# Kernel optimization log

Hardware: AMD Instinct MI355X
Metric: run time of the kernel (lower is better)

The kernel has to match this reference:

```python
import jax, jax.numpy as jnp
import numpy as np

B, N, C, H, K = 16, 2048, 64, 128, 16
EPS = 1e-5  # torch BatchNorm1d default eps


def _bn(h, g, b, axes):
    # training-mode batch norm: biased variance over all non-channel axes
    m = h.mean(axes, keepdims=True)
    v = h.var(axes, keepdims=True)
    return (h - m) * jax.lax.rsqrt(v + EPS) * g + b


def _edge_conv(x, W1, b1, g1, be1, W2, b2, g2, be2):
    # x: [B, N, C]; dynamic kNN graph in feature space (per graph), includes self
    sq = jnp.sum(x * x, axis=-1)                                   # [B, N]
    d2 = sq[:, :, None] + sq[:, None, :] - 2.0 * jnp.einsum('bnc,bmc->bnm', x, x)
    idx = jax.lax.top_k(-d2, K)[1]                                 # [B, N, K]
    xj = jax.vmap(lambda xb, ib: xb[ib])(x, idx)                   # [B, N, K, C]
    xi = jnp.broadcast_to(x[:, :, None, :], xj.shape)
    h = jnp.concatenate([xi, xj - xi], axis=-1) @ W1 + b1          # [B, N, K, H]
    h = jax.nn.relu(_bn(h, g1, be1, (0, 1, 2)))
    h = h @ W2 + b2
    h = jax.nn.relu(_bn(h, g2, be2, (0, 1, 2)))
    return h.max(axis=2)                                           # max aggregation -> [B, N, H]


def setup_inputs() -> dict:
    key = jax.random.key(0)
    ks = jax.random.split(key, 8)
    inp = {
        'x': jax.random.normal(ks[0], (B * N, C), jnp.float32),
        'batch': jnp.repeat(jnp.arange(B, dtype=jnp.int32), N),
    }
    i = 1
    for pref in ('s', 't'):
        inp[f'{pref}_W1'] = jax.random.normal(ks[i], (2 * C, H), jnp.float32) * 0.05; i += 1
        inp[f'{pref}_b1'] = jnp.zeros((H,), jnp.float32)
        inp[f'{pref}_g1'] = jnp.ones((H,), jnp.float32)
        inp[f'{pref}_be1'] = jnp.zeros((H,), jnp.float32)
        inp[f'{pref}_W2'] = jax.random.normal(ks[i], (H, H), jnp.float32) * 0.05; i += 1
        inp[f'{pref}_b2'] = jnp.zeros((H,), jnp.float32)
        inp[f'{pref}_g2'] = jnp.ones((H,), jnp.float32)
        inp[f'{pref}_be2'] = jnp.zeros((H,), jnp.float32)
    inp['f_W'] = jax.random.normal(ks[i], (2 * H, H), jnp.float32) * 0.05
    inp['f_b'] = jnp.zeros((H,), jnp.float32)
    inp['f_g'] = jnp.ones((H,), jnp.float32)
    inp['f_be'] = jnp.zeros((H,), jnp.float32)
    return inp


def reference(x, batch,
              s_W1, s_b1, s_g1, s_be1, s_W2, s_b2, s_g2, s_be2,
              t_W1, t_b1, t_g1, t_be1, t_W2, t_b2, t_g2, t_be2,
              f_W, f_b, f_g, f_be):
    # batch is sorted with B equal-size graphs of N nodes -> reshape
    xb = x.reshape(B, N, C)
    xs = _edge_conv(xb, s_W1, s_b1, s_g1, s_be1, s_W2, s_b2, s_g2, s_be2)
    xt = _edge_conv(xb, t_W1, t_b1, t_g1, t_be1, t_W2, t_b2, t_g2, t_be2)
    comb = jnp.concatenate([xs, xt], axis=-1).reshape(B * N, 2 * H)
    h = comb @ f_W + f_b
    return jax.nn.relu(_bn(h, f_g, f_be, (0,)))
```

## Files before the change

### kernel.cpp

```cpp
#include <hip/hip_runtime.h>
#include <hip/hip_bf16.h>
#include <stdint.h>

#define NB 16
#define NN 2048
#define NC 64
#define NH 128
#define NK 16
#define NS (NB*NN)
#define NSK (NS*NK)
#define EPSV 1e-5f

typedef __attribute__((ext_vector_type(8))) short short8;
typedef __attribute__((ext_vector_type(8))) _Float16 half8;
typedef __attribute__((ext_vector_type(8))) unsigned short ushort8;
typedef __attribute__((ext_vector_type(4))) float f32x4;

__device__ __forceinline__ unsigned short f2bf(float x) {
  union { float f; unsigned u; } v; v.f = x;
  unsigned r = v.u + 0x7fffu + ((v.u >> 16) & 1u);
  return (unsigned short)(r >> 16);
}

__device__ __forceinline__ unsigned orderf(float f) {
  unsigned u = __float_as_uint(f);
  return u ^ ((unsigned)((int)u >> 31) | 0x80000000u);
}

__device__ __forceinline__ unsigned long long shfl_xor_u64(unsigned long long v, int m) {
  unsigned lo = (unsigned)(v & 0xffffffffull);
  unsigned hi = (unsigned)(v >> 32);
  lo = __shfl_xor(lo, m, 64);
  hi = __shfl_xor(hi, m, 64);
  return (((unsigned long long)hi) << 32) | lo;
}

__global__ void prep_x(const float* __restrict__ x, float* __restrict__ sq,
                       unsigned short* __restrict__ xh, unsigned short* __restrict__ xl) {
  int i = blockIdx.x * blockDim.x + threadIdx.x;
  if (i >= NS) return;
  const float4* x4 = (const float4*)(x + (size_t)i * NC);
  float s = 0.f;
#pragma unroll
  for (int k = 0; k < 8; k++) {
    float4 a = x4[2*k], b = x4[2*k+1];
    float f[8] = {a.x,a.y,a.z,a.w,b.x,b.y,b.z,b.w};
    ushort8 hv, lv;
#pragma unroll
    for (int j = 0; j < 8; j++) {
      float v = f[j];
      s += v*v;
      _Float16 h = (_Float16)v;
      float r = v - (float)h;
      _Float16 l = (_Float16)r;
      union { _Float16 ff; unsigned short u; } ch, cl;
      ch.ff = h; cl.ff = l;
      hv[j] = ch.u; lv[j] = cl.u;
    }
    *(ushort8*)(xh + (size_t)i*64 + k*8) = hv;
    *(ushort8*)(xl + (size_t)i*64 + k*8) = lv;
  }
  sq[i] = s;
}

__global__ __launch_bounds__(256) void knn5_kernel(const unsigned short* __restrict__ xh,
                                                   const unsigned short* __restrict__ xl,
                                                   const float* __restrict__ sq,
                                                   int* __restrict__ nbr) {
  __shared__ unsigned short rAh[64*64], rAl[64*64];
  __shared__ unsigned short cBh[64*64], cBl[64*64];
  __shared__ float sqc[64];
  __shared__ float d2s[256*17];
  int b = blockIdx.x >> 5;
  int rb = blockIdx.x & 31;
  int w = threadIdx.x >> 6, lane = threadIdx.x & 63;
  int n16 = lane & 15, q = lane >> 4;
  int rowbase = b*NN + rb*64;
  float* myd2 = &d2s[threadIdx.x * 17];

  {
    int r = threadIdx.x >> 2;
    int c0 = (threadIdx.x & 3) * 2;
#pragma unroll
    for (int cc = 0; cc < 2; cc++) {
      int c = c0 + cc;
      int pos = (c ^ (r & 7)) * 8;
      *(ushort8*)&rAh[r*64 + pos] = *(const ushort8*)(xh + (size_t)(rowbase + r)*64 + c*8);
      *(ushort8*)&rAl[r*64 + pos] = *(const ushort8*)(xl + (size_t)(rowbase + r)*64 + c*8);
    }
  }
  __syncthreads();
  half8 bh[2], bl[2];
  int m = w*16 + n16;
#pragma unroll
  for (int ks = 0; ks < 2; ks++) {
    int pos = ((ks*4 + q) ^ (m & 7)) * 8;
    bh[ks] = *(const half8*)&rAh[m*64 + pos];
    bl[ks] = *(const half8*)&rAl[m*64 + pos];
  }
  float sqr = sq[rowbase + m];

  unsigned long long keys[16];
#pragma unroll
  for (int i = 0; i < 16; i++) keys[i] = ~0ull;
  float wd2 = __builtin_inff();

  for (int ch = 0; ch < 32; ch++) {
    int colbase = b*NN + ch*64;
    __syncthreads();
    {
      int r = threadIdx.x >> 2;
      int c0 = (threadIdx.x & 3) * 2;
#pragma unroll
      for (int cc = 0; cc < 2; cc++) {
        int c = c0 + cc;
        int pos = (c ^ (r & 7)) * 8;
        *(ushort8*)&cBh[r*64 + pos] = *(const ushort8*)(xh + (size_t)(colbase + r)*64 + c*8);
        *(ushort8*)&cBl[r*64 + pos] = *(const ushort8*)(xl + (size_t)(colbase + r)*64 + c*8);
      }
      if (threadIdx.x < 64) sqc[threadIdx.x] = sq[colbase + threadIdx.x];
    }
    __syncthreads();
    f32x4 acc[4];
#pragma unroll
    for (int ci = 0; ci < 4; ci++) acc[ci] = (f32x4){0.f,0.f,0.f,0.f};
#pragma unroll
    for (int ks = 0; ks < 2; ks++) {
#pragma unroll
      for (int ci = 0; ci < 4; ci++) {
        int n = ci*16 + n16;
        int pos = ((ks*4 + q) ^ (n & 7)) * 8;
        half8 ah_ = *(const half8*)&cBh[n*64 + pos];
        half8 al_ = *(const half8*)&cBl[n*64 + pos];
        acc[ci] = __builtin_amdgcn_mfma_f32_16x16x32_f16(ah_, bh[ks], acc[ci], 0, 0, 0);
        acc[ci] = __builtin_amdgcn_mfma_f32_16x16x32_f16(al_, bh[ks], acc[ci], 0, 0, 0);
        acc[ci] = __builtin_amdgcn_mfma_f32_16x16x32_f16(ah_, bl[ks], acc[ci], 0, 0, 0);
      }
    }
    unsigned mask = 0;
#pragma unroll
    for (int ci = 0; ci < 4; ci++)
#pragma unroll
      for (int r = 0; r < 4; r++) {
        int idx = ci*4 + r;
        float d2 = fmaf(-2.f, acc[ci][r], sqr + sqc[ci*16 + q*4 + r]);
        myd2[idx] = d2;
        mask |= (d2 <= wd2) ? (1u << idx) : 0u;
      }
    while (mask) {
      int i = __builtin_ctz(mask);
      mask &= mask - 1;
      float dd = myd2[i];
      if (dd > wd2) continue;
      int col = colbase + (i >> 2)*16 + q*4 + (i & 3);
      unsigned long long key = ((unsigned long long)orderf(dd) << 32) | (unsigned)col;
#pragma unroll
      for (int j = 0; j < 16; j++) {
        bool cl = key < keys[j];
        unsigned long long lo = cl ? key : keys[j];
        key = cl ? keys[j] : key;
        keys[j] = lo;
      }
      unsigned whi = (unsigned)(keys[15] >> 32);
      wd2 = (whi == 0xffffffffu) ? __builtin_inff()
          : __uint_as_float((whi & 0x80000000u) ? (whi ^ 0x80000000u) : ~whi);
    }
  }
  for (int j = 0; j < NK; j++) {
    unsigned long long mk = keys[0];
#pragma unroll
    for (int i = 1; i < 16; i++) mk = (keys[i] < mk) ? keys[i] : mk;
    unsigned long long o = shfl_xor_u64(mk, 16); mk = (o < mk) ? o : mk;
    o = shfl_xor_u64(mk, 32); mk = (o < mk) ? o : mk;
#pragma unroll
    for (int i = 0; i < 16; i++) if (keys[i] == mk) keys[i] = ~0ull;
    if (q == 0) nbr[(size_t)(rowbase + m)*NK + j] = (int)(mk & 0xffffffffu);
  }
}

__global__ void prep_weights(const float* __restrict__ sW1, const float* __restrict__ sW2,
                             const float* __restrict__ tW1, const float* __restrict__ tW2,
                             const float* __restrict__ fW,
                             unsigned short* __restrict__ sW1t, unsigned short* __restrict__ sW2t,
                             unsigned short* __restrict__ tW1t, unsigned short* __restrict__ tW2t,
                             unsigned short* __restrict__ fWt) {
  int i = blockIdx.x * blockDim.x + threadIdx.x;
  if (i < 4*16384) {
    int mi = i >> 14, e = i & 16383;
    int h = e >> 7, k = e & 127;
    const float* src = (mi==0) ? sW1 : (mi==1) ? sW2 : (mi==2) ? tW1 : tW2;
    unsigned short* dst = (mi==0) ? sW1t : (mi==1) ? sW2t : (mi==2) ? tW1t : tW2t;
    dst[h*128 + k] = f2bf(src[k*128 + h]);
  } else {
    int e = i - 4*16384;
    if (e < 128*256) {
      int h = e >> 8, k = e & 255;
      fWt[h*256 + k] = f2bf(fW[k*128 + h]);
    }
  }
}

__global__ __launch_bounds__(256) void pnode_kernel(
    const float* __restrict__ x,
    const unsigned short* __restrict__ sW1t, const unsigned short* __restrict__ tW1t,
    float* __restrict__ PS, float* __restrict__ PT) {
  __shared__ unsigned short xt_[64*64];
  int rowbase = blockIdx.x * 64;
  int lane = threadIdx.x & 63;
  int wave = threadIdx.x >> 6;
  int n16 = lane & 15, q = lane >> 4;
  int cb = wave * 32;
  {
    int r = threadIdx.x >> 2, part = threadIdx.x & 3;
    const float4* xp = (const float4*)(x + (size_t)(rowbase + r) * NC) + part*4;
#pragma unroll
    for (int cc = 0; cc < 2; cc++) {
      int c = part*2 + cc;
      float4 a = xp[cc*2], b = xp[cc*2+1];
      int pos = (c ^ (r & 7)) * 8;
      unsigned short* d = &xt_[r*64 + pos];
      d[0]=f2bf(a.x); d[1]=f2bf(a.y); d[2]=f2bf(a.z); d[3]=f2bf(a.w);
      d[4]=f2bf(b.x); d[5]=f2bf(b.y); d[6]=f2bf(b.z); d[7]=f2bf(b.w);
    }
  }
  __syncthreads();
  f32x4 aS[4][2], aT[4][2];
#pragma unroll
  for (int ri = 0; ri < 4; ri++)
#pragma unroll
    for (int ci = 0; ci < 2; ci++) {
      aS[ri][ci] = (f32x4){0.f,0.f,0.f,0.f};
      aT[ri][ci] = (f32x4){0.f,0.f,0.f,0.f};
    }
#pragma unroll
  for (int ks = 0; ks < 2; ks++) {
    short8 af[4];
#pragma unroll
    for (int ri = 0; ri < 4; ri++) {
      int m = ri*16 + n16;
      af[ri] = *(const short8*)&xt_[m*64 + (((ks*4+q) ^ (m & 7)))*8];
    }
#pragma unroll
    for (int ci = 0; ci < 2; ci++) {
      int col = cb + ci*16 + n16;
      short8 bS = *(const short8*)(sW1t + col*128 + (ks*4+q)*8);
      short8 bT = *(const short8*)(tW1t + col*128 + (ks*4+q)*8);
#pragma unroll
      for (int ri = 0; ri < 4; ri++) {
        aS[ri][ci] = __builtin_amdgcn_mfma_f32_16x16x32_bf16(af[ri], bS, aS[ri][ci], 0, 0, 0);
        aT[ri][ci] = __builtin_amdgcn_mfma_f32_16x16x32_bf16(af[ri], bT, aT[ri][ci], 0, 0, 0);
      }
    }
  }
#pragma unroll
  for (int ri = 0; ri < 4; ri++)
#pragma unroll
    for (int ci = 0; ci < 2; ci++) {
      int col = cb + ci*16 + n16;
#pragma unroll
      for (int r = 0; r < 4; r++) {
        int row = rowbase + ri*16 + q*4 + r;
        PS[(size_t)row*128 + col] = aS[ri][ci][r];
        PT[(size_t)row*128 + col] = aT[ri][ci][r];
      }
    }
}

__global__ __launch_bounds__(256, 2) void dstat_kernel(
    const float* __restrict__ x, const int* __restrict__ nbr,
    const unsigned short* __restrict__ sW1t, const unsigned short* __restrict__ tW1t,
    const float* __restrict__ PS, const float* __restrict__ PT,
    unsigned short* __restrict__ D,
    float* __restrict__ statS, float* __restrict__ statT) {
  __shared__ unsigned short dlds[64*64];
  int wave = threadIdx.x >> 6, lane = threadIdx.x & 63;
  int n16 = lane & 15, q = lane >> 4;
  int cb = wave * 32;
  int g = blockIdx.x & 15, sub = blockIdx.x >> 4;
  float psS[2]={0,0}, ps2S[2]={0,0}, psT[2]={0,0}, ps2T[2]={0,0};

  for (int it = 0; it < 4; it++) {
    int tile = g*512 + sub*4 + it;
    __syncthreads();
    {
      int r4 = threadIdx.x >> 2, part = threadIdx.x & 3;
      int s = tile*64 + r4;
      int node = s >> 4;
      int ng = nbr[s];
      const float4* xi = (const float4*)(x + (size_t)node * NC) + part*4;
      const float4* xj = (const float4*)(x + (size_t)ng  * NC) + part*4;
      unsigned short* dstg = D + (size_t)tile*4096 + (size_t)r4*64;
#pragma unroll
      for (int cc = 0; cc < 2; cc++) {
        int c = part*2 + cc;
        float4 a0 = xi[cc*2], a1 = xi[cc*2+1];
        float4 b0 = xj[cc*2], b1 = xj[cc*2+1];
        int pos = (c ^ (r4 & 7)) * 8;
        ushort8 dv;
        dv[0]=f2bf(b0.x-a0.x); dv[1]=f2bf(b0.y-a0.y); dv[2]=f2bf(b0.z-a0.z); dv[3]=f2bf(b0.w-a0.w);
        dv[4]=f2bf(b1.x-a1.x); dv[5]=f2bf(b1.y-a1.y); dv[6]=f2bf(b1.z-a1.z); dv[7]=f2bf(b1.w-a1.w);
        *(ushort8*)(dstg + pos) = dv;
        *(ushort8*)(dlds + r4*64 + pos) = dv;
      }
    }
    __syncthreads();
    int node0 = tile*4;
    float pS[4][2], pT[4][2];
#pragma unroll
    for (int ri = 0; ri < 4; ri++)
#pragma unroll
      for (int ci = 0; ci < 2; ci++) {
        int col = cb + ci*16 + n16;
        pS[ri][ci] = PS[(size_t)(node0+ri)*128 + col];
        pT[ri][ci] = PT[(size_t)(node0+ri)*128 + col];
      }
    f32x4 aS[4][2], aT[4][2];
#pragma unroll
    for (int ri = 0; ri < 4; ri++)
#pragma unroll
      for (int ci = 0; ci < 2; ci++) {
        aS[ri][ci] = (f32x4){0.f,0.f,0.f,0.f};
        aT[ri][ci] = (f32x4){0.f,0.f,0.f,0.f};
      }
#pragma unroll
    for (int ks = 0; ks < 2; ks++) {
      short8 af[4];
#pragma unroll
      for (int ri = 0; ri < 4; ri++) {
        int m = ri*16 + n16;
        af[ri] = *(const short8*)&dlds[m*64 + ((ks*4+q) ^ (m & 7))*8];
      }
#pragma unroll
      for (int ci = 0; ci < 2; ci++) {
        int col = cb + ci*16 + n16;
        short8 bS = *(const short8*)(sW1t + col*128 + 64 + (ks*4+q)*8);
        short8 bT = *(const short8*)(tW1t + col*128 + 64 + (ks*4+q)*8);
#pragma unroll
        for (int ri = 0; ri < 4; ri++) {
          aS[ri][ci] = __builtin_amdgcn_mfma_f32_16x16x32_bf16(af[ri], bS, aS[ri][ci], 0, 0, 0);
          aT[ri][ci] = __builtin_amdgcn_mfma_f32_16x16x32_bf16(af[ri], bT, aT[ri][ci], 0, 0, 0);
        }
      }
    }
#pragma unroll
    for (int ci = 0; ci < 2; ci++)
#pragma unroll
      for (int ri = 0; ri < 4; ri++)
#pragma unroll
        for (int r = 0; r < 4; r++) {
          float vS = aS[ri][ci][r] + pS[ri][ci];
          float vT = aT[ri][ci][r] + pT[ri][ci];
          psS[ci] += vS; ps2S[ci] += vS*vS;
          psT[ci] += vT; ps2T[ci] += vT*vT;
        }
  }
#pragma unroll
  for (int ci = 0; ci < 2; ci++) {
    int col = cb + ci*16 + n16;
    float a = psS[ci], a2 = ps2S[ci], b2v = psT[ci], b3 = ps2T[ci];
    a   += __shfl_xor(a, 16, 64);   a   += __shfl_xor(a, 32, 64);
    a2  += __shfl_xor(a2, 16, 64);  a2  += __shfl_xor(a2, 32, 64);
    b2v += __shfl_xor(b2v, 16, 64); b2v += __shfl_xor(b2v, 32, 64);
    b3  += __shfl_xor(b3, 16, 64);  b3  += __shfl_xor(b3, 32, 64);
    if (q == 0) {
      atomicAdd(&statS[col], a);
      atomicAdd(&statS[128 + col], a2);
      atomicAdd(&statT[col], b2v);
      atomicAdd(&statT[128 + col], b3);
    }
  }
}

template<int MODE>
__global__ __launch_bounds__(256, 2) void mlp_pass2(
    const unsigned short* __restrict__ D,
    const float* __restrict__ PS, const float* __restrict__ PT,
    const unsigned short* __restrict__ sW1t, const unsigned short* __restrict__ sW2t,
    const unsigned short* __restrict__ tW1t, const unsigned short* __restrict__ tW2t,
    const unsigned short* __restrict__ fWt,
    const float* __restrict__ affS1, const float* __restrict__ affS2,
    const float* __restrict__ affT1, const float* __restrict__ affT2,
    float* __restrict__ statS, float* __restrict__ statT,
    float* __restrict__ statF, float* __restrict__ gout) {
  __shared__ unsigned short dlds[64*64];
  __shared__ unsigned short atile[64*128];
  __shared__ unsigned short xtile[(MODE == 2) ? 16*256 : 64];
  int wave = threadIdx.x >> 6;
  int lane = threadIdx.x & 63;
  int n16 = lane & 15, q = lane >> 4;
  int cb = wave * 32;

  float s1S[2], h1S[2], s2S[2], h2S[2];
  float s1T[2], h1T[2], s2T[2], h2T[2];
#pragma unroll
  for (int ci = 0; ci < 2; ci++) {
    int col = cb + ci*16 + n16;
    s1S[ci] = affS1[col]; h1S[ci] = affS1[128 + col];
    s1T[ci] = affT1[col]; h1T[ci] = affT1[128 + col];
  }
  if (MODE == 2) {
#pragma unroll
    for (int ci = 0; ci < 2; ci++) {
      int col = cb + ci*16 + n16;
      s2S[ci] = affS2[col]; h2S[ci] = affS2[128 + col];
      s2T[ci] = affT2[col]; h2T[ci] = affT2[128 + col];
    }
  }
  float psS[2] = {0,0}, ps2S[2] = {0,0};
  float psT[2] = {0,0}, ps2T[2] = {0,0};

  for (int it = 0; it < 4; it++) {
    int tile = blockIdx.x*4 + it;
    __syncthreads();
    {
      const ushort8* src = (const ushort8*)(D + (size_t)tile*4096);
      ushort8* dst = (ushort8*)dlds;
      dst[threadIdx.x] = src[threadIdx.x];
      dst[threadIdx.x + 256] = src[threadIdx.x + 256];
    }
    __syncthreads();
    int node0 = tile*4;
    float pS[4][2], pT[4][2];
#pragma unroll
    for (int ri = 0; ri < 4; ri++)
#pragma unroll
      for (int ci = 0; ci < 2; ci++) {
        int col = cb + ci*16 + n16;
        pS[ri][ci] = PS[(size_t)(node0+ri)*128 + col];
        pT[ri][ci] = PT[(size_t)(node0+ri)*128 + col];
      }

#pragma unroll
    for (int st = 0; st < 2; st++) {
      const unsigned short* W1t = st ? tW1t : sW1t;
      const unsigned short* W2t = st ? tW2t : sW2t;
      const float* sc1 = st ? s1T : s1S;  const float* sh1 = st ? h1T : h1S;
      const float* sc2 = st ? s2T : s2S;  const float* sh2 = st ? h2T : h2S;
      float (*pp)[2] = st ? pT : pS;
      float* ps  = st ? psT : psS;
      float* ps2 = st ? ps2T : ps2S;

      f32x4 acc[4][2];
#pragma unroll
      for (int ri = 0; ri < 4; ri++)
#pragma unroll
        for (int ci = 0; ci < 2; ci++)
          acc[ri][ci] = (f32x4){0.f,0.f,0.f,0.f};
#pragma unroll
      for (int ks = 0; ks < 2; ks++) {
        short8 af[4], bf[2];
#pragma unroll
        for (int ri = 0; ri < 4; ri++) {
          int mm = ri*16 + n16;
          af[ri] = *(const short8*)&dlds[mm*64 + ((ks*4+q) ^ (mm & 7))*8];
        }
#pragma unroll
        for (int ci = 0; ci < 2; ci++) {
          int col = cb + ci*16 + n16;
          bf[ci] = *(const short8*)(W1t + col*128 + 64 + (ks*4+q)*8);
        }
#pragma unroll
        for (int ri = 0; ri < 4; ri++)
#pragma unroll
          for (int ci = 0; ci < 2; ci++)
            acc[ri][ci] = __builtin_amdgcn_mfma_f32_16x16x32_bf16(af[ri], bf[ci], acc[ri][ci], 0, 0, 0);
      }
#pragma unroll
      for (int ri = 0; ri < 4; ri++)
#pragma unroll
        for (int ci = 0; ci < 2; ci++) {
          int colL = cb + ci*16 + n16;
          int kc8 = colL >> 3;
#pragma unroll
          for (int r = 0; r < 4; r++) {
            float v = acc[ri][ci][r] + pp[ri][ci];
            v = fmaxf(v * sc1[ci] + sh1[ci], 0.f);
            int rowL = ri*16 + q*4 + r;
            int pos = ((kc8 ^ (rowL & 7)) << 3) + (colL & 7);
            atile[rowL*128 + pos] = f2bf(v);
          }
        }
      __syncthreads();
      f32x4 acc2[4][2];
#pragma unroll
      for (int ri = 0; ri < 4; ri++)
#pragma unroll
        for (int ci = 0; ci < 2; ci++)
          acc2[ri][ci] = (f32x4){0.f,0.f,0.f,0.f};
#pragma unroll
      for (int ks = 0; ks < 4; ks++) {
        short8 a2[4], bf[2];
#pragma unroll
        for (int ri = 0; ri < 4; ri++) {
          int mm = ri*16 + n16;
          int kc8 = (ks*4 + q) ^ (mm & 7);
          a2[ri] = *(const short8*)&atile[mm*128 + kc8*8];
        }
#pragma unroll
        for (int ci = 0; ci < 2; ci++) {
          int col = cb + ci*16 + n16;
          bf[ci] = *(const short8*)(W2t + col*128 + ks*32 + q*8);
        }
#pragma unroll
        for (int ri = 0; ri < 4; ri++)
#pragma unroll
          for (int ci = 0; ci < 2; ci++)
            acc2[ri][ci] = __builtin_amdgcn_mfma_f32_16x16x32_bf16(a2[ri], bf[ci], acc2[ri][ci], 0, 0, 0);
      }
      if (MODE == 1) {
#pragma unroll
        for (int ci = 0; ci < 2; ci++)
#pragma unroll
          for (int ri = 0; ri < 4; ri++)
#pragma unroll
            for (int r = 0; r < 4; r++) {
              float v = acc2[ri][ci][r];
              ps[ci] += v; ps2[ci] += v*v;
            }
      } else {
#pragma unroll
        for (int ri = 0; ri < 4; ri++)
#pragma unroll
          for (int ci = 0; ci < 2; ci++) {
            int col = cb + ci*16 + n16;
            float vm = 0.f;
#pragma unroll
            for (int r = 0; r < 4; r++) {
              float v = fmaxf(acc2[ri][ci][r] * sc2[ci] + sh2[ci], 0.f);
              vm = fmaxf(vm, v);
            }
            vm = fmaxf(vm, __shfl_xor(vm, 16, 64));
            vm = fmaxf(vm, __shfl_xor(vm, 32, 64));
            if (q == 0) {
              int ln = it*4 + ri;
              int fcol = st*128 + col;
              int kc8 = fcol >> 3;
              int pos = ((kc8 ^ (ln & 7)) << 3) + (fcol & 7);
              xtile[ln*256 + pos] = f2bf(vm);
            }
          }
      }
      if (st == 0) __syncthreads();
    }
  }
  if (MODE == 1) {
#pragma unroll
    for (int ci = 0; ci < 2; ci++) {
      int col = cb + ci*16 + n16;
      float a = psS[ci], a2 = ps2S[ci], b = psT[ci], b2 = ps2T[ci];
      a  += __shfl_xor(a, 16, 64);  a  += __shfl_xor(a, 32, 64);
      a2 += __shfl_xor(a2, 16, 64); a2 += __shfl_xor(a2, 32, 64);
      b  += __shfl_xor(b, 16, 64);  b  += __shfl_xor(b, 32, 64);
      b2 += __shfl_xor(b2, 16, 64); b2 += __shfl_xor(b2, 32, 64);
      if (q == 0) {
        atomicAdd(&statS[col], a);
        atomicAdd(&statS[128 + col], a2);
        atomicAdd(&statT[col], b);
        atomicAdd(&statT[128 + col], b2);
      }
    }
  } else {
    __syncthreads();
    f32x4 facc[2];
#pragma unroll
    for (int ci = 0; ci < 2; ci++) facc[ci] = (f32x4){0.f,0.f,0.f,0.f};
#pragma unroll
    for (int ks = 0; ks < 8; ks++) {
      int kc8 = (ks*4 + q) ^ (n16 & 7);
      short8 af = *(const short8*)&xtile[n16*256 + kc8*8];
#pragma unroll
      for (int ci = 0; ci < 2; ci++) {
        int col = cb + ci*16 + n16;
        short8 bf = *(const short8*)(fWt + col*256 + ks*32 + q*8);
        facc[ci] = __builtin_amdgcn_mfma_f32_16x16x32_bf16(af, bf, facc[ci], 0, 0, 0);
      }
    }
    int nodeBase = blockIdx.x * 16;
    float fs[2] = {0,0}, fs2[2] = {0,0};
#pragma unroll
    for (int ci = 0; ci < 2; ci++) {
      int col = cb + ci*16 + n16;
#pragma unroll
      for (int r = 0; r < 4; r++) {
        float v = facc[ci][r];
        gout[(size_t)(nodeBase + q*4 + r)*128 + col] = v;
        fs[ci] += v; fs2[ci] += v*v;
      }
      float a = fs[ci], a2 = fs2[ci];
      a  += __shfl_xor(a, 16, 64);  a  += __shfl_xor(a, 32, 64);
      a2 += __shfl_xor(a2, 16, 64); a2 += __shfl_xor(a2, 32, 64);
      if (q == 0) {
        atomicAdd(&statF[col], a);
        atomicAdd(&statF[128 + col], a2);
      }
    }
  }
}

__global__ void finalize_kernel(const float* __restrict__ stats,
                                const float* __restrict__ g,
                                const float* __restrict__ be,
                                float* __restrict__ aff, float invcount) {
  int c = threadIdx.x;
  if (c < 128) {
    float mean = stats[c] * invcount;
    float var = stats[128 + c] * invcount - mean*mean;
    float scale = g[c] / sqrtf(var + EPSV);
    aff[c] = scale;
    aff[128 + c] = be[c] - mean * scale;
  }
}

__global__ void apply_bn_kernel(float* __restrict__ out, const float* __restrict__ aff) {
  int i = blockIdx.x * blockDim.x + threadIdx.x;
  if (i < NS*NH) {
    int c = i & 127;
    out[i] = fmaxf(out[i] * aff[c] + aff[128 + c], 0.f);
  }
}

extern "C" void kernel_launch(void* const* d_in, const int* in_sizes, int n_in,
                              void* d_out, int out_size, void* d_ws, size_t ws_size,
                              hipStream_t stream) {
  const float* x   = (const float*)d_in[0];
  const float* sW1 = (const float*)d_in[2];
  const float* sg1 = (const float*)d_in[4];
  const float* sbe1= (const float*)d_in[5];
  const float* sW2 = (const float*)d_in[6];
  const float* sg2 = (const float*)d_in[8];
  const float* sbe2= (const float*)d_in[9];
  const float* tW1 = (const float*)d_in[10];
  const float* tg1 = (const float*)d_in[12];
  const float* tbe1= (const float*)d_in[13];
  const float* tW2 = (const float*)d_in[14];
  const float* tg2 = (const float*)d_in[16];
  const float* tbe2= (const float*)d_in[17];
  const float* fW  = (const float*)d_in[18];
  const float* fg  = (const float*)d_in[20];
  const float* fbe = (const float*)d_in[21];
  float* out = (float*)d_out;

  char* w = (char*)d_ws;
  float* sq = (float*)w;                 w += (size_t)NS*4;
  int* nbr = (int*)w;                    w += (size_t)NSK*4;
  unsigned short* sW1t = (unsigned short*)w; w += 32768;
  unsigned short* sW2t = (unsigned short*)w; w += 32768;
  unsigned short* tW1t = (unsigned short*)w; w += 32768;
  unsigned short* tW2t = (unsigned short*)w; w += 32768;
  unsigned short* fWt  = (unsigned short*)w; w += 65536;
  float* stats = (float*)w;              w += 2560*4;
  unsigned short* xh = (unsigned short*)w; w += (size_t)NS*64*2;
  unsigned short* xl = (unsigned short*)w; w += (size_t)NS*64*2;
  unsigned short* Dg = (unsigned short*)w; w += (size_t)NSK*64*2;
  float* PS = (float*)w;                 w += (size_t)NS*128*4;
  float* PT = (float*)w;                 w += (size_t)NS*128*4;

  float* st_s1 = stats;        float* af_s1 = stats + 256;
  float* st_s2 = stats + 512;  float* af_s2 = stats + 768;
  float* st_t1 = stats + 1024; float* af_t1 = stats + 1280;
  float* st_t2 = stats + 1536; float* af_t2 = stats + 1792;
  float* st_f  = stats + 2048; float* af_f  = stats + 2304;

  hipMemsetAsync(stats, 0, 2560*4, stream);
  prep_weights<<<(4*16384 + 128*256 + 255)/256, 256, 0, stream>>>(
      sW1, sW2, tW1, tW2, fW, sW1t, sW2t, tW1t, tW2t, fWt);
  prep_x<<<NS/256, 256, 0, stream>>>(x, sq, xh, xl);
  knn5_kernel<<<NB*32, 256, 0, stream>>>(xh, xl, sq, nbr);
  pnode_kernel<<<NS/64, 256, 0, stream>>>(x, sW1t, tW1t, PS, PT);
  dstat_kernel<<<2048, 256, 0, stream>>>(x, nbr, sW1t, tW1t, PS, PT, Dg, st_s1, st_t1);

  const float inv1 = 1.f/(float)NSK, invf = 1.f/(float)NS;
  finalize_kernel<<<1,128,0,stream>>>(st_s1, sg1, sbe1, af_s1, inv1);
  finalize_kernel<<<1,128,0,stream>>>(st_t1, tg1, tbe1, af_t1, inv1);
  mlp_pass2<1><<<2048,256,0,stream>>>(Dg, PS, PT, sW1t, sW2t, tW1t, tW2t, fWt,
      af_s1, nullptr, af_t1, nullptr, st_s2, st_t2, nullptr, nullptr);
  finalize_kernel<<<1,128,0,stream>>>(st_s2, sg2, sbe2, af_s2, inv1);
  finalize_kernel<<<1,128,0,stream>>>(st_t2, tg2, tbe2, af_t2, inv1);
  mlp_pass2<2><<<2048,256,0,stream>>>(Dg, PS, PT, sW1t, sW2t, tW1t, tW2t, fWt,
      af_s1, af_s2, af_t1, af_t2, nullptr, nullptr, st_f, out);
  finalize_kernel<<<1,128,0,stream>>>(st_f, fg, fbe, af_f, invf);
  apply_bn_kernel<<<(NS*NH)/256, 256, 0, stream>>>(out, af_f);
}
```

Baseline: 573.0 us.

## Split kNN column range across two blocks per row tile and merge partial top-k

The kNN kernel now launches twice as many blocks, each scanning half of the candidate columns for a 64-row tile and writing its sorted partial top-16 keys to a temporary buffer. A new merge kernel combines the two sorted lists per row into the final neighbour indices. This is meant to fill more compute units, since the previous 512-block grid was small for the GPU. The per-thread LDS distance staging is also dropped in favour of keeping distances in registers and reading sqc as float4. The cost is an extra kernel launch and a global round trip of 8 MB of partial keys.

Result: slower. 646.9 us (+12.9%).

```diff
diff --git a/kernel.cpp b/kernel.cpp
--- a/kernel.cpp
+++ b/kernel.cpp
@@ -63,20 +63,18 @@
   sq[i] = s;
 }
 
-__global__ __launch_bounds__(256) void knn5_kernel(const unsigned short* __restrict__ xh,
+__global__ __launch_bounds__(256) void knn6_kernel(const unsigned short* __restrict__ xh,
                                                    const unsigned short* __restrict__ xl,
                                                    const float* __restrict__ sq,
-                                                   int* __restrict__ nbr) {
+                                                   unsigned long long* __restrict__ tmpk) {
   __shared__ unsigned short rAh[64*64], rAl[64*64];
   __shared__ unsigned short cBh[64*64], cBl[64*64];
-  __shared__ float sqc[64];
-  __shared__ float d2s[256*17];
-  int b = blockIdx.x >> 5;
-  int rb = blockIdx.x & 31;
+  __shared__ __align__(16) float sqc[64];
+  int rblock = blockIdx.x >> 1, half = blockIdx.x & 1;
+  int b = rblock >> 5, rb = rblock & 31;
   int w = threadIdx.x >> 6, lane = threadIdx.x & 63;
   int n16 = lane & 15, q = lane >> 4;
   int rowbase = b*NN + rb*64;
-  float* myd2 = &d2s[threadIdx.x * 17];
 
   {
     int r = threadIdx.x >> 2;
@@ -105,7 +103,7 @@
   for (int i = 0; i < 16; i++) keys[i] = ~0ull;
   float wd2 = __builtin_inff();
 
-  for (int ch = 0; ch < 32; ch++) {
+  for (int ch = half*16; ch < half*16 + 16; ch++) {
     int colbase = b*NN + ch*64;
     __syncthreads();
     {
@@ -137,33 +135,36 @@
         acc[ci] = __builtin_amdgcn_mfma_f32_16x16x32_f16(ah_, bl[ks], acc[ci], 0, 0, 0);
       }
     }
-    unsigned mask = 0;
-#pragma unroll
-    for (int ci = 0; ci < 4; ci++)
-#pragma unroll
-      for (int r = 0; r < 4; r++) {
-        int idx = ci*4 + r;
-        float d2 = fmaf(-2.f, acc[ci][r], sqr + sqc[ci*16 + q*4 + r]);
-        myd2[idx] = d2;
-        mask |= (d2 <= wd2) ? (1u << idx) : 0u;
-      }
-    while (mask) {
-      int i = __builtin_ctz(mask);
-      mask &= mask - 1;
-      float dd = myd2[i];
-      if (dd > wd2) continue;
-      int col = colbase + (i >> 2)*16 + q*4 + (i & 3);
-      unsigned long long key = ((unsigned long long)orderf(dd) << 32) | (unsigned)col;
-#pragma unroll
-      for (int j = 0; j < 16; j++) {
-        bool cl = key < keys[j];
-        unsigned long long lo = cl ? key : keys[j];
-        key = cl ? keys[j] : key;
-        keys[j] = lo;
-      }
-      unsigned whi = (unsigned)(keys[15] >> 32);
-      wd2 = (whi == 0xffffffffu) ? __builtin_inff()
-          : __uint_as_float((whi & 0x80000000u) ? (whi ^ 0x80000000u) : ~whi);
+#pragma unroll
+    for (int ci = 0; ci < 4; ci++) {
+      f32x4 s4 = *(const f32x4*)&sqc[ci*16 + q*4];
+      float d0 = fmaf(-2.f, acc[ci][0], sqr + s4[0]);
+      float d1 = fmaf(-2.f, acc[ci][1], sqr + s4[1]);
+      float d2_ = fmaf(-2.f, acc[ci][2], sqr + s4[2]);
+      float d3 = fmaf(-2.f, acc[ci][3], sqr + s4[3]);
+      unsigned m4 = 0;
+      m4 |= (d0 <= wd2) ? 1u : 0u;
+      m4 |= (d1 <= wd2) ? 2u : 0u;
+      m4 |= (d2_ <= wd2) ? 4u : 0u;
+      m4 |= (d3 <= wd2) ? 8u : 0u;
+      while (m4) {
+        int r = __builtin_ctz(m4);
+        m4 &= m4 - 1;
+        float dd = (r & 2) ? ((r & 1) ? d3 : d2_) : ((r & 1) ? d1 : d0);
+        if (dd > wd2) continue;
+        int col = colbase + ci*16 + q*4 + r;
+        unsigned long long key = ((unsigned long long)orderf(dd) << 32) | (unsigned)col;
+#pragma unroll
+        for (int j = 0; j < 16; j++) {
+          bool cl = key < keys[j];
+          unsigned long long lo = cl ? key : keys[j];
+          key = cl ? keys[j] : key;
+          keys[j] = lo;
+        }
+        unsigned whi = (unsigned)(keys[15] >> 32);
+        wd2 = (whi == 0xffffffffu) ? __builtin_inff()
+            : __uint_as_float((whi & 0x80000000u) ? (whi ^ 0x80000000u) : ~whi);
+      }
     }
   }
   for (int j = 0; j < NK; j++) {
@@ -174,7 +175,24 @@
     o = shfl_xor_u64(mk, 32); mk = (o < mk) ? o : mk;
 #pragma unroll
     for (int i = 0; i < 16; i++) if (keys[i] == mk) keys[i] = ~0ull;
-    if (q == 0) nbr[(size_t)(rowbase + m)*NK + j] = (int)(mk & 0xffffffffu);
+    if (q == 0) tmpk[((size_t)(rowbase + m)*2 + half)*16 + j] = mk;
+  }
+}
+
+__global__ void knn_merge_kernel(const unsigned long long* __restrict__ tmpk,
+                                 int* __restrict__ nbr) {
+  int row = blockIdx.x * 256 + threadIdx.x;
+  if (row >= NS) return;
+  const unsigned long long* A = tmpk + (size_t)row*32;
+  const unsigned long long* B = A + 16;
+  int ia = 0, ib = 0;
+  unsigned long long ka = A[0], kb = B[0];
+#pragma unroll
+  for (int j = 0; j < 16; j++) {
+    bool ta = ka <= kb;
+    nbr[(size_t)row*16 + j] = (int)((ta ? ka : kb) & 0xffffffffu);
+    if (ta) { ia++; ka = (ia < 16) ? A[ia] : ~0ull; }
+    else    { ib++; kb = (ib < 16) ? B[ib] : ~0ull; }
   }
 }
 
@@ -654,6 +672,7 @@
   unsigned short* Dg = (unsigned short*)w; w += (size_t)NSK*64*2;
   float* PS = (float*)w;                 w += (size_t)NS*128*4;
   float* PT = (float*)w;                 w += (size_t)NS*128*4;
+  unsigned long long* tmpk = (unsigned long long*)w; w += (size_t)NS*32*8;
 
   float* st_s1 = stats;        float* af_s1 = stats + 256;
   float* st_s2 = stats + 512;  float* af_s2 = stats + 768;
@@ -665,7 +684,8 @@
   prep_weights<<<(4*16384 + 128*256 + 255)/256, 256, 0, stream>>>(
       sW1, sW2, tW1, tW2, fW, sW1t, sW2t, tW1t, tW2t, fWt);
   prep_x<<<NS/256, 256, 0, stream>>>(x, sq, xh, xl);
-  knn5_kernel<<<NB*32, 256, 0, stream>>>(xh, xl, sq, nbr);
+  knn6_kernel<<<NB*32*2, 256, 0, stream>>>(xh, xl, sq, tmpk);
+  knn_merge_kernel<<<NS/256, 256, 0, stream>>>(tmpk, nbr);
   pnode_kernel<<<NS/64, 256, 0, stream>>>(x, sW1t, tW1t, PS, PT);
   dstat_kernel<<<2048, 256, 0, stream>>>(x, nbr, sW1t, tW1t, PS, PT, Dg, st_s1, st_t1);
 
```

## Share kNN threshold across lanes and raise occupancy of MLP kernels

Applied to the files above, without the earlier changes.

In the kNN kernel, each quad lane group now takes the minimum of its per-lane worst top-K distance via shuffles, so all four lanes of a row prune with the tightest known threshold. The LDS spill of distances is also skipped when no candidate passes. The dstat kernel processes the S and T branches one after the other instead of interleaving them, which halves live accumulator registers. dstat and mlp_pass2 launch bounds are raised from 2 to 4 blocks per CU. The higher occupancy target risks register spills, especially in mlp_pass2, which was otherwise left unchanged.

Result: slower. 869.8 us (+51.8%).

```diff
diff --git a/kernel.cpp b/kernel.cpp
--- a/kernel.cpp
+++ b/kernel.cpp
@@ -25,6 +25,11 @@
 __device__ __forceinline__ unsigned orderf(float f) {
   unsigned u = __float_as_uint(f);
   return u ^ ((unsigned)((int)u >> 31) | 0x80000000u);
+}
+
+__device__ __forceinline__ float unorderf(unsigned whi) {
+  return (whi == 0xffffffffu) ? __builtin_inff()
+       : __uint_as_float((whi & 0x80000000u) ? (whi ^ 0x80000000u) : ~whi);
 }
 
 __device__ __forceinline__ unsigned long long shfl_xor_u64(unsigned long long v, int m) {
@@ -137,6 +142,7 @@
         acc[ci] = __builtin_amdgcn_mfma_f32_16x16x32_f16(ah_, bl[ks], acc[ci], 0, 0, 0);
       }
     }
+    float d2v[16];
     unsigned mask = 0;
 #pragma unroll
     for (int ci = 0; ci < 4; ci++)
@@ -144,26 +150,34 @@
       for (int r = 0; r < 4; r++) {
         int idx = ci*4 + r;
         float d2 = fmaf(-2.f, acc[ci][r], sqr + sqc[ci*16 + q*4 + r]);
-        myd2[idx] = d2;
+        d2v[idx] = d2;
         mask |= (d2 <= wd2) ? (1u << idx) : 0u;
       }
-    while (mask) {
-      int i = __builtin_ctz(mask);
-      mask &= mask - 1;
-      float dd = myd2[i];
-      if (dd > wd2) continue;
-      int col = colbase + (i >> 2)*16 + q*4 + (i & 3);
-      unsigned long long key = ((unsigned long long)orderf(dd) << 32) | (unsigned)col;
-#pragma unroll
-      for (int j = 0; j < 16; j++) {
-        bool cl = key < keys[j];
-        unsigned long long lo = cl ? key : keys[j];
-        key = cl ? keys[j] : key;
-        keys[j] = lo;
-      }
+    if (mask) {
+#pragma unroll
+      for (int i = 0; i < 16; i++) myd2[i] = d2v[i];
+      while (mask) {
+        int i = __builtin_ctz(mask);
+        mask &= mask - 1;
+        float dd = myd2[i];
+        if (dd > wd2) continue;
+        int col = colbase + (i >> 2)*16 + q*4 + (i & 3);
+        unsigned long long key = ((unsigned long long)orderf(dd) << 32) | (unsigned)col;
+#pragma unroll
+        for (int j = 0; j < 16; j++) {
+          bool cl = key < keys[j];
+          unsigned long long lo = cl ? key : keys[j];
+          key = cl ? keys[j] : key;
+          keys[j] = lo;
+        }
+        wd2 = fminf(wd2, unorderf((unsigned)(keys[15] >> 32)));
+      }
+    }
+    {
       unsigned whi = (unsigned)(keys[15] >> 32);
-      wd2 = (whi == 0xffffffffu) ? __builtin_inff()
-          : __uint_as_float((whi & 0x80000000u) ? (whi ^ 0x80000000u) : ~whi);
+      unsigned o = __shfl_xor(whi, 16, 64); whi = (o < whi) ? o : whi;
+      o = __shfl_xor(whi, 32, 64); whi = (o < whi) ? o : whi;
+      wd2 = unorderf(whi);
     }
   }
   for (int j = 0; j < NK; j++) {
@@ -266,7 +280,7 @@
     }
 }
 
-__global__ __launch_bounds__(256, 2) void dstat_kernel(
+__global__ __launch_bounds__(256, 4) void dstat_kernel(
     const float* __restrict__ x, const int* __restrict__ nbr,
     const unsigned short* __restrict__ sW1t, const unsigned short* __restrict__ tW1t,
     const float* __restrict__ PS, const float* __restrict__ PT,
@@ -305,54 +319,51 @@
     }
     __syncthreads();
     int node0 = tile*4;
-    float pS[4][2], pT[4][2];
-#pragma unroll
-    for (int ri = 0; ri < 4; ri++)
-#pragma unroll
-      for (int ci = 0; ci < 2; ci++) {
-        int col = cb + ci*16 + n16;
-        pS[ri][ci] = PS[(size_t)(node0+ri)*128 + col];
-        pT[ri][ci] = PT[(size_t)(node0+ri)*128 + col];
-      }
-    f32x4 aS[4][2], aT[4][2];
-#pragma unroll
-    for (int ri = 0; ri < 4; ri++)
-#pragma unroll
-      for (int ci = 0; ci < 2; ci++) {
-        aS[ri][ci] = (f32x4){0.f,0.f,0.f,0.f};
-        aT[ri][ci] = (f32x4){0.f,0.f,0.f,0.f};
-      }
-#pragma unroll
-    for (int ks = 0; ks < 2; ks++) {
-      short8 af[4];
-#pragma unroll
-      for (int ri = 0; ri < 4; ri++) {
-        int m = ri*16 + n16;
-        af[ri] = *(const short8*)&dlds[m*64 + ((ks*4+q) ^ (m & 7))*8];
-      }
-#pragma unroll
-      for (int ci = 0; ci < 2; ci++) {
-        int col = cb + ci*16 + n16;
-        short8 bS = *(const short8*)(sW1t + col*128 + 64 + (ks*4+q)*8);
-        short8 bT = *(const short8*)(tW1t + col*128 + 64 + (ks*4+q)*8);
+#pragma unroll
+    for (int st = 0; st < 2; st++) {
+      const unsigned short* W1t = st ? tW1t : sW1t;
+      const float* P = st ? PT : PS;
+      float* ps  = st ? psT : psS;
+      float* ps2 = st ? ps2T : ps2S;
+      float pp[4][2];
+#pragma unroll
+      for (int ri = 0; ri < 4; ri++)
+#pragma unroll
+        for (int ci = 0; ci < 2; ci++)
+          pp[ri][ci] = P[(size_t)(node0+ri)*128 + cb + ci*16 + n16];
+      f32x4 a[4][2];
+#pragma unroll
+      for (int ri = 0; ri < 4; ri++)
+#pragma unroll
+        for (int ci = 0; ci < 2; ci++)
+          a[ri][ci] = (f32x4){0.f,0.f,0.f,0.f};
+#pragma unroll
+      for (int ks = 0; ks < 2; ks++) {
+        short8 af[4];
 #pragma unroll
         for (int ri = 0; ri < 4; ri++) {
-          aS[ri][ci] = __builtin_amdgcn_mfma_f32_16x16x32_bf16(af[ri], bS, aS[ri][ci], 0, 0, 0);
-          aT[ri][ci] = __builtin_amdgcn_mfma_f32_16x16x32_bf16(af[ri], bT, aT[ri][ci], 0, 0, 0);
-        }
-      }
-    }
-#pragma unroll
-    for (int ci = 0; ci < 2; ci++)
-#pragma unroll
-      for (int ri = 0; ri < 4; ri++)
-#pragma unroll
-        for (int r = 0; r < 4; r++) {
-          float vS = aS[ri][ci][r] + pS[ri][ci];
-          float vT = aT[ri][ci][r] + pT[ri][ci];
-          psS[ci] += vS; ps2S[ci] += vS*vS;
-          psT[ci] += vT; ps2T[ci] += vT*vT;
-        }
+          int mm = ri*16 + n16;
+          af[ri] = *(const short8*)&dlds[mm*64 + ((ks*4+q) ^ (mm & 7))*8];
+        }
+#pragma unroll
+        for (int ci = 0; ci < 2; ci++) {
+          int col = cb + ci*16 + n16;
+          short8 bf = *(const short8*)(W1t + col*128 + 64 + (ks*4+q)*8);
+#pragma unroll
+          for (int ri = 0; ri < 4; ri++)
+            a[ri][ci] = __builtin_amdgcn_mfma_f32_16x16x32_bf16(af[ri], bf, a[ri][ci], 0, 0, 0);
+        }
+      }
+#pragma unroll
+      for (int ci = 0; ci < 2; ci++)
+#pragma unroll
+        for (int ri = 0; ri < 4; ri++)
+#pragma unroll
+          for (int r = 0; r < 4; r++) {
+            float v = a[ri][ci][r] + pp[ri][ci];
+            ps[ci] += v; ps2[ci] += v*v;
+          }
+    }
   }
 #pragma unroll
   for (int ci = 0; ci < 2; ci++) {
@@ -372,7 +383,7 @@
 }
 
 template<int MODE>
-__global__ __launch_bounds__(256, 2) void mlp_pass2(
+__global__ __launch_bounds__(256, 4) void mlp_pass2(
     const unsigned short* __restrict__ D,
     const float* __restrict__ PS, const float* __restrict__ PT,
     const unsigned short* __restrict__ sW1t, const unsigned short* __restrict__ sW2t,
```
